# Kernel tuning notes

Hardware: AMD Instinct MI355X
Metric: run time of the kernel (lower is better)

## Reference

```python
import jax, jax.numpy as jnp
import numpy as np

B, CIN, COUT, R = 8, 256, 256, 128  # H = W = R (required by the module's permute-then-conv structure)


def _init_linear(key, out_c, in_c):
    # mimic torch Conv2d(kernel=1) default init: uniform(-1/sqrt(fan_in), 1/sqrt(fan_in))
    k1, k2 = jax.random.split(key)
    bound = 1.0 / np.sqrt(in_c)
    W = jax.random.uniform(k1, (out_c, in_c), jnp.float32, -bound, bound)
    b = jax.random.uniform(k2, (out_c,), jnp.float32, -bound, bound)
    return W, b


def setup_inputs() -> dict:
    key = jax.random.key(0)
    keys = jax.random.split(key, 9)
    x = jax.random.normal(keys[0], (B, CIN, R, R), jnp.float32)
    Wr, br = _init_linear(keys[1], R, CIN)          # resize conv
    Wqw, bqw = _init_linear(keys[2], R, R)          # width-attn q (mixes over H axis, H==R)
    Wkw, bkw = _init_linear(keys[3], R, R)
    Wvw, bvw = _init_linear(keys[4], R, R)
    Wqh, bqh = _init_linear(keys[5], R, R)          # height-attn q (mixes over W axis, W==R)
    Wkh, bkh = _init_linear(keys[6], R, R)
    Wvh, bvh = _init_linear(keys[7], R, R)
    Wo, bo = _init_linear(keys[8], COUT, R)         # restore conv
    return dict(x=x, Wr=Wr, br=br, Wqw=Wqw, bqw=bqw, Wkw=Wkw, bkw=bkw, Wvw=Wvw, bvw=bvw,
                Wqh=Wqh, bqh=bqh, Wkh=Wkh, bkh=bkh, Wvh=Wvh, bvh=bvh, Wo=Wo, bo=bo)


def _csaa_forward(x, Wr, br, Wqw, bqw, Wkw, bkw, Wvw, bvw, Wqh, bqh, Wkh, bkh, Wvh, bvh, Wo, bo):
    # resize 1x1 conv: [B,CIN,H,W] -> [B,R,H,W]
    resized = jnp.einsum('oc,bchw->bohw', Wr, x) + br[None, :, None, None]

    # --- width-branch AxialAttention (height_dim=False) ---
    # permute(0,2,1,3): [B,R,H,W] -> [B,H,R,W]; 1x1 conv now mixes over the H axis (H==R)
    xp = jnp.transpose(resized, (0, 2, 1, 3))                      # [B,H,R,W]
    q = jnp.einsum('oh,bhrw->borw', Wqw, xp) + bqw[None, :, None, None]
    k = jnp.einsum('oh,bhrw->borw', Wkw, xp) + bkw[None, :, None, None]
    v = jnp.einsum('oh,bhrw->borw', Wvw, xp) + bvw[None, :, None, None]
    attn = jax.nn.softmax(jnp.einsum('borw,bouw->boru', q, k), axis=-1)  # [B,O,R,R]
    out = jnp.einsum('boru,bouw->borw', attn, v)                   # [B,O,R,W]
    w_attn = jnp.transpose(out, (0, 2, 1, 3))                      # [B,R,O,W] == [B,R,H,W]

    # --- height-branch AxialAttention (height_dim=True) ---
    # permute(0,3,1,2): [B,R,H,W] -> [B,W,R,H]; 1x1 conv mixes over the W axis (W==R)
    xp = jnp.transpose(w_attn, (0, 3, 1, 2))                       # [B,W,R,H]
    q = jnp.einsum('ow,bwrh->borh', Wqh, xp) + bqh[None, :, None, None]
    k = jnp.einsum('ow,bwrh->borh', Wkh, xp) + bkh[None, :, None, None]
    v = jnp.einsum('ow,bwrh->borh', Wvh, xp) + bvh[None, :, None, None]
    attn = jax.nn.softmax(jnp.einsum('borh,bouh->boru', q, k), axis=-1)  # [B,O,R,R]
    out = jnp.einsum('boru,bouh->borh', attn, v)                   # [B,O,R,H]
    h_attn = jnp.transpose(out, (0, 2, 3, 1))                      # [B,R,H,O] == [B,R,H,W]

    # restore 1x1 conv: [B,R,H,W] -> [B,COUT,H,W]
    return jnp.einsum('oc,bchw->bohw', Wo, h_attn) + bo[None, :, None, None]


def reference(x, Wr, br, Wqw, bqw, Wkw, bkw, Wvw, bvw, Wqh, bqh, Wkh, bkh, Wvh, bvh, Wo, bo):
    return _csaa_forward(x, Wr, br, Wqw, bqw, Wkw, bkw, Wvw, bvw,
                         Wqh, bqh, Wkh, bkh, Wvh, bvh, Wo, bo)
```

## Files before the change

kernel.cpp:

```cpp
#include <hip/hip_runtime.h>
#include <hip/hip_bf16.h>


typedef __attribute__((ext_vector_type(8))) short bf16x8;
typedef __attribute__((ext_vector_type(4))) float f32x4;

__device__ __forceinline__ short f2b(float f) {
    __hip_bfloat16 h = __float2bfloat16(f);
    short s; __builtin_memcpy(&s, &h, 2);
    return s;
}

__device__ __forceinline__ int swx(int row) { return (row ^ (row >> 3)) & 7; }
__device__ __forceinline__ int swzb(int row, int blk) {
    return (row << 7) + ((blk ^ swx(row)) << 3);
}

__device__ __forceinline__ void gload16(const void* g, void* l) {
    __builtin_amdgcn_global_load_lds(
        (const __attribute__((address_space(1))) void*)g,
        (__attribute__((address_space(3))) void*)l, 16, 0, 0);
}

__device__ __forceinline__ void mfma_ag(const short* __restrict__ Ai,
                                        const short* __restrict__ Bs,
                                        f32x4 (&acc)[2][8], int lane, int wr) {
    #pragma unroll
    for (int kk = 0; kk < 4; kk++) {
        const int kb = kk * 4 + (lane >> 4);
        bf16x8 a[2];
        #pragma unroll
        for (int mi = 0; mi < 2; mi++)
            a[mi] = *(const bf16x8*)(Ai + kb * 1024
                                        + (wr + mi * 16 + (lane & 15)) * 8);
        #pragma unroll
        for (int nh = 0; nh < 2; nh++) {
            bf16x8 b[4];
            #pragma unroll
            for (int nj = 0; nj < 4; nj++)
                b[nj] = *(const bf16x8*)&Bs[swzb((nh * 4 + nj) * 16 + (lane & 15), kb)];
            #pragma unroll
            for (int mi = 0; mi < 2; mi++)
                #pragma unroll
                for (int nj = 0; nj < 4; nj++)
                    acc[mi][nh * 4 + nj] = __builtin_amdgcn_mfma_f32_16x16x32_bf16(
                        a[mi], b[nj], acc[mi][nh * 4 + nj], 0, 0, 0);
        }
    }
}

__device__ __forceinline__ void mfma16x128(const short* __restrict__ SA,
                                           const short* __restrict__ SB,
                                           f32x4 (&acc)[8], int lane, int wr16) {
    #pragma unroll
    for (int kk = 0; kk < 4; kk++) {
        const int kb = kk * 4 + (lane >> 4);
        bf16x8 a = *(const bf16x8*)&SA[swzb(wr16 + (lane & 15), kb)];
        #pragma unroll
        for (int nh = 0; nh < 2; nh++) {
            bf16x8 b[4];
            #pragma unroll
            for (int nj = 0; nj < 4; nj++)
                b[nj] = *(const bf16x8*)&SB[swzb((nh * 4 + nj) * 16 + (lane & 15), kb)];
            #pragma unroll
            for (int nj = 0; nj < 4; nj++)
                acc[nh * 4 + nj] = __builtin_amdgcn_mfma_f32_16x16x32_bf16(
                    a, b[nj], acc[nh * 4 + nj], 0, 0, 0);
        }
    }
}

__device__ __forceinline__ void mfma32x128(const short* __restrict__ SA,
                                           const short* __restrict__ SB,
                                           f32x4 (&acc)[2][8], int lane, int wr) {
    #pragma unroll
    for (int kk = 0; kk < 4; kk++) {
        const int kb = kk * 4 + (lane >> 4);
        bf16x8 a[2], b[8];
        #pragma unroll
        for (int mi = 0; mi < 2; mi++)
            a[mi] = *(const bf16x8*)&SA[swzb(wr + mi * 16 + (lane & 15), kb)];
        #pragma unroll
        for (int ni = 0; ni < 8; ni++)
            b[ni] = *(const bf16x8*)&SB[swzb(ni * 16 + (lane & 15), kb)];
        #pragma unroll
        for (int mi = 0; mi < 2; mi++)
            #pragma unroll
            for (int ni = 0; ni < 8; ni++)
                acc[mi][ni] = __builtin_amdgcn_mfma_f32_16x16x32_bf16(
                    a[mi], b[ni], acc[mi][ni], 0, 0, 0);
    }
}

__device__ __forceinline__ void stage_nf_bf16(const short* __restrict__ Bb,
                                              long long b_r, int k0,
                                              short* __restrict__ Bs, int t) {
    const int n8 = t & 15, kb = t >> 4;
    bf16x8 rk[8];
    #pragma unroll
    for (int i = 0; i < 8; i++)
        rk[i] = *(const bf16x8*)(Bb + (long long)(k0 + kb * 8 + i) * b_r + n8 * 8);
    #pragma unroll
    for (int j = 0; j < 8; j++) {
        bf16x8 col;
        #pragma unroll
        for (int i = 0; i < 8; i++) col[i] = rk[i][j];
        *(bf16x8*)&Bs[swzb(n8 * 8 + j, kb)] = col;
    }
}

__device__ __forceinline__ void stage_nf_f32(const float* __restrict__ Bb,
                                             long long b_r, int k0,
                                             short* __restrict__ Bs, int t) {
    const int n8 = t & 15, kb = t >> 4;
    bf16x8 rk[8];
    #pragma unroll
    for (int i = 0; i < 8; i++) {
        const float* s = Bb + (long long)(k0 + kb * 8 + i) * b_r + n8 * 8;
        float4 v0 = *(const float4*)s, v1 = *(const float4*)(s + 4);
        rk[i][0] = f2b(v0.x); rk[i][1] = f2b(v0.y);
        rk[i][2] = f2b(v0.z); rk[i][3] = f2b(v0.w);
        rk[i][4] = f2b(v1.x); rk[i][5] = f2b(v1.y);
        rk[i][6] = f2b(v1.z); rk[i][7] = f2b(v1.w);
    }
    #pragma unroll
    for (int j = 0; j < 8; j++) {
        bf16x8 col;
        #pragma unroll
        for (int i = 0; i < 8; i++) col[i] = rk[i][j];
        *(bf16x8*)&Bs[swzb(n8 * 8 + j, kb)] = col;
    }
}

__global__ __launch_bounds__(256)
void wprep(const float* __restrict__ Wr, const float* __restrict__ Wqw,
           const float* __restrict__ Wkw, const float* __restrict__ Wvw,
           const float* __restrict__ Wqh, const float* __restrict__ Wkh,
           const float* __restrict__ Wvh, const float* __restrict__ Wo,
           short* __restrict__ dst) {
    const int id = blockIdx.y;
    const float* W; int M, K, off;
    switch (id) {
        case 0: W = Wr;  M = 128; K = 256; off = 0;      break;
        case 1: W = Wqw; M = 128; K = 128; off = 32768;  break;
        case 2: W = Wkw; M = 128; K = 128; off = 49152;  break;
        case 3: W = Wvw; M = 128; K = 128; off = 65536;  break;
        case 4: W = Wqh; M = 128; K = 128; off = 81920;  break;
        case 5: W = Wkh; M = 128; K = 128; off = 98304;  break;
        case 6: W = Wvh; M = 128; K = 128; off = 114688; break;
        default: W = Wo; M = 256; K = 128; off = 131072; break;
    }
    int g = blockIdx.x * 256 + threadIdx.x;
    if (g >= (M * K) >> 3) return;
    int gpr = K >> 3;
    int row = g / gpr;
    int blk = g - row * gpr;
    int ks = blk >> 4, kb = blk & 15;
    int my = row >> 7, r = row & 127;
    int nks = K >> 7;
    const float* s = W + (long long)row * K + blk * 8;
    float4 v0 = *(const float4*)s, v1 = *(const float4*)(s + 4);
    bf16x8 ov;
    ov[0] = f2b(v0.x); ov[1] = f2b(v0.y); ov[2] = f2b(v0.z); ov[3] = f2b(v0.w);
    ov[4] = f2b(v1.x); ov[5] = f2b(v1.y); ov[6] = f2b(v1.z); ov[7] = f2b(v1.w);
    *(bf16x8*)(dst + off + ((my * nks + ks) * 16 + kb) * 1024 + r * 8) = ov;
}

__global__ __launch_bounds__(256, 4)
void gemm_p1(const short* __restrict__ A0, const float* __restrict__ bias0,
             const float* __restrict__ Bsrc,
             long long b_z, long long b_x, long long b_r,
             short* __restrict__ C0,
             long long c_z, long long c_x, long long c_m) {
    __shared__ short Bs[16384];
    const int t = threadIdx.x;
    const int lane = t & 63;
    const int wid = t >> 6;
    const int wr = wid * 32;
    const int bx = blockIdx.x, bz = blockIdx.z;

    f32x4 acc[2][8];
    #pragma unroll
    for (int mi = 0; mi < 2; mi++)
        #pragma unroll
        for (int ni = 0; ni < 8; ni++) acc[mi][ni] = (f32x4){0.f, 0.f, 0.f, 0.f};

    #pragma unroll
    for (int ks = 0; ks < 2; ks++) {
        if (ks) __syncthreads();
        stage_nf_f32(Bsrc + bz * b_z + bx * b_x, b_r, ks * 128, Bs, t);
        __syncthreads();
        mfma_ag(A0 + ks * 16384, Bs, acc, lane, wr);
    }
    __syncthreads();

    #pragma unroll
    for (int mi = 0; mi < 2; mi++)
        #pragma unroll
        for (int r = 0; r < 4; r++) {
            int row = wr + mi * 16 + (lane >> 4) * 4 + r;
            float bb = bias0[row];
            #pragma unroll
            for (int ni = 0; ni < 8; ni++) {
                int col = ni * 16 + (lane & 15);
                Bs[swzb(row, col >> 3) + (col & 7)] = f2b(acc[mi][ni][r] + bb);
            }
        }
    short* Cg = C0 + bz * c_z + bx * c_x;
    #pragma unroll
    for (int i = 0; i < 8; i++) {
        int idx = lane + i * 64;
        int row = wr + (idx >> 4), ch = idx & 15;
        *(bf16x8*)(Cg + (long long)row * c_m + ch * 8) =
            *(const bf16x8*)&Bs[swzb(row, ch)];
    }
}

template<int NW, int BMODE, bool F32OUT>
__global__ __launch_bounds__(256, 4)
void gemmu(const short* __restrict__ A0, const short* __restrict__ A1,
           const short* __restrict__ A2,
           const float* __restrict__ bias0, const float* __restrict__ bias1,
           const float* __restrict__ bias2,
           const void* __restrict__ Bsrc, long long b_z, long long b_x,
           long long b_r,
           short* __restrict__ C0, short* __restrict__ C1,
           short* __restrict__ C2, float* __restrict__ Cf,
           long long c_z, long long c_x, long long c_m) {
    __shared__ short Bs[16384];
    const int t = threadIdx.x;
    const int lane = t & 63;
    const int wid = t >> 6;
    const int wr = wid * 32;
    const int bx = blockIdx.x, gy = blockIdx.y, bz = blockIdx.z;

    const short* Ai;
    const float* bias;
    int myoff;
    if (NW > 1) {
        Ai = (gy == 0) ? A0 : (gy == 1) ? A1 : A2;
        bias = (gy == 0) ? bias0 : (gy == 1) ? bias1 : bias2;
        myoff = 0;
    } else {
        Ai = A0 + gy * 16384;
        bias = bias0;
        myoff = gy * 128;
    }

    if (BMODE == 0) {
        const short* Bb = (const short*)Bsrc + bz * b_z + bx * b_x;
        #pragma unroll
        for (int i = 0; i < 8; i++) {
            int q = wid * 8 + i;
            int row = q * 4 + (lane >> 4);
            gload16(Bb + (long long)row * b_r + (((lane & 15) ^ swx(row)) << 3),
                    &Bs[q * 512]);
        }
    } else {
        stage_nf_bf16((const short*)Bsrc + bz * b_z + bx * b_x, b_r, 0, Bs, t);
    }
    __syncthreads();

    f32x4 acc[2][8];
    #pragma unroll
    for (int mi = 0; mi < 2; mi++)
        #pragma unroll
        for (int ni = 0; ni < 8; ni++) acc[mi][ni] = (f32x4){0.f, 0.f, 0.f, 0.f};
    mfma_ag(Ai, Bs, acc, lane, wr);

    if (F32OUT) {
        float* Cb = Cf + bz * c_z + bx * c_x;
        #pragma unroll
        for (int mi = 0; mi < 2; mi++)
            #pragma unroll
            for (int r = 0; r < 4; r++) {
                int row = myoff + wr + mi * 16 + (lane >> 4) * 4 + r;
                float bb = bias[row];
                float* cp = Cb + (long long)row * c_m + (lane & 15);
                #pragma unroll
                for (int ni = 0; ni < 8; ni++)
                    cp[ni * 16] = acc[mi][ni][r] + bb;
            }
    } else {
        __syncthreads();
        #pragma unroll
        for (int mi = 0; mi < 2; mi++)
            #pragma unroll
            for (int r = 0; r < 4; r++) {
                int row = wr + mi * 16 + (lane >> 4) * 4 + r;
                float bb = bias[row];
                #pragma unroll
                for (int ni = 0; ni < 8; ni++) {
                    int col = ni * 16 + (lane & 15);
                    Bs[swzb(row, col >> 3) + (col & 7)] = f2b(acc[mi][ni][r] + bb);
                }
            }
        short* Cg = ((NW > 1) ? ((gy == 0) ? C0 : (gy == 1) ? C1 : C2) : C0)
                  + bz * c_z + bx * c_x;
        #pragma unroll
        for (int i = 0; i < 8; i++) {
            int idx = lane + i * 64;
            int row = wr + (idx >> 4), ch = idx & 15;
            *(bf16x8*)(Cg + (long long)row * c_m + ch * 8) =
                *(const bf16x8*)&Bs[swzb(row, ch)];
        }
    }
}

__global__ __launch_bounds__(256, 3)
void attnq(const short* __restrict__ Q, const short* __restrict__ Kp,
           const short* __restrict__ V, short* __restrict__ O) {
    __shared__ short SA[8192];
    __shared__ short SB[16384];
    const int t = threadIdx.x;
    const int lane = t & 63;
    const int wid = t >> 6;
    const int wr16 = wid * 16;
    const int o = blockIdx.x, qh = blockIdx.y, b = blockIdx.z;
    const long long poff = (long long)b * 2097152LL + (long long)o * 16384LL;
    const short* Qb = Q + poff + qh * 64 * 128;
    const short* Kb = Kp + poff;
    const short* Vb = V + poff;
    short* Ob = O + (long long)b * 2097152LL + (long long)o * 128LL
              + (long long)qh * 64 * 16384LL;

    #pragma unroll
    for (int i = 0; i < 4; i++) {
        int q = wid * 4 + i;
        int row = q * 4 + (lane >> 4);
        gload16(Qb + row * 128 + (((lane & 15) ^ swx(row)) << 3), &SA[q * 512]);
    }
    #pragma unroll
    for (int i = 0; i < 8; i++) {
        int q = wid * 8 + i;
        int row = q * 4 + (lane >> 4);
        gload16(Kb + row * 128 + (((lane & 15) ^ swx(row)) << 3), &SB[q * 512]);
    }
    const int n8 = t & 15, kb8 = t >> 4;
    bf16x8 vk[8];
    #pragma unroll
    for (int i = 0; i < 8; i++)
        vk[i] = *(const bf16x8*)(Vb + (kb8 * 8 + i) * 128 + n8 * 8);
    __syncthreads();

    f32x4 acc[8];
    #pragma unroll
    for (int ni = 0; ni < 8; ni++) acc[ni] = (f32x4){0.f, 0.f, 0.f, 0.f};
    mfma16x128(SA, SB, acc, lane, wr16);

    float rs[4];
    #pragma unroll
    for (int r = 0; r < 4; r++) {
        float mx = acc[0][r];
        #pragma unroll
        for (int ni = 1; ni < 8; ni++) mx = fmaxf(mx, acc[ni][r]);
        #pragma unroll
        for (int d = 1; d < 16; d <<= 1) mx = fmaxf(mx, __shfl_xor(mx, d, 64));
        float s = 0.f, p[8];
        #pragma unroll
        for (int ni = 0; ni < 8; ni++) {
            p[ni] = __expf(acc[ni][r] - mx);
            s += p[ni];
        }
        #pragma unroll
        for (int d = 1; d < 16; d <<= 1) s += __shfl_xor(s, d, 64);
        rs[r] = 1.f / s;
        int row = wr16 + (lane >> 4) * 4 + r;
        #pragma unroll
        for (int ni = 0; ni < 8; ni++) {
            int col = ni * 16 + (lane & 15);
            SA[swzb(row, col >> 3) + (col & 7)] = f2b(p[ni]);
        }
    }
    __syncthreads();

    #pragma unroll
    for (int j = 0; j < 8; j++) {
        bf16x8 col;
        #pragma unroll
        for (int i = 0; i < 8; i++) col[i] = vk[i][j];
        *(bf16x8*)&SB[swzb(n8 * 8 + j, kb8)] = col;
    }
    __syncthreads();

    f32x4 acc2[8];
    #pragma unroll
    for (int ni = 0; ni < 8; ni++) acc2[ni] = (f32x4){0.f, 0.f, 0.f, 0.f};
    mfma16x128(SA, SB, acc2, lane, wr16);

    #pragma unroll
    for (int r = 0; r < 4; r++) {
        int row = wr16 + (lane >> 4) * 4 + r;
        float rinv = rs[r];
        #pragma unroll
        for (int ni = 0; ni < 8; ni++) {
            int col = ni * 16 + (lane & 15);
            SA[swzb(row, col >> 3) + (col & 7)] = f2b(acc2[ni][r] * rinv);
        }
    }
    #pragma unroll
    for (int i = 0; i < 4; i++) {
        int idx = lane + i * 64;
        int row = wr16 + (idx >> 4), ch = idx & 15;
        *(bf16x8*)(Ob + (long long)row * 16384 + ch * 8) =
            *(const bf16x8*)&SA[swzb(row, ch)];
    }
}

template<bool TEPI>
__global__ __launch_bounds__(256)
void attnk(const short* __restrict__ Q, const short* __restrict__ Kp,
           const short* __restrict__ V, short* __restrict__ O) {
    __shared__ short SA[16384];
    __shared__ short SB[16384];
    const int t = threadIdx.x;
    const int lane = t & 63;
    const int wid = t >> 6;
    const int wr = wid * 32;
    const long long poff = (long long)blockIdx.z * 2097152LL
                         + (long long)blockIdx.x * 16384LL;
    const short* Qb = Q + poff;
    const short* Kb = Kp + poff;
    const short* Vb = V + poff;
    short* Ob = O + (long long)blockIdx.z * 2097152LL + (long long)blockIdx.x * 128LL;

    #pragma unroll
    for (int i = 0; i < 8; i++) {
        int q = wid * 8 + i;
        int row = q * 4 + (lane >> 4);
        int sw = (((lane & 15) ^ swx(row)) << 3);
        gload16(Qb + row * 128 + sw, &SA[q * 512]);
        gload16(Kb + row * 128 + sw, &SB[q * 512]);
    }
    const int n8 = t & 15, kb = t >> 4;
    bf16x8 vk[8];
    #pragma unroll
    for (int i = 0; i < 8; i++)
        vk[i] = *(const bf16x8*)(Vb + (kb * 8 + i) * 128 + n8 * 8);
    __syncthreads();

    f32x4 acc[2][8];
    #pragma unroll
    for (int mi = 0; mi < 2; mi++)
        #pragma unroll
        for (int ni = 0; ni < 8; ni++) acc[mi][ni] = (f32x4){0.f, 0.f, 0.f, 0.f};
    mfma32x128(SA, SB, acc, lane, wr);

    float rs[2][4];
    #pragma unroll
    for (int mi = 0; mi < 2; mi++)
        #pragma unroll
        for (int r = 0; r < 4; r++) {
            float mx = acc[mi][0][r];
            #pragma unroll
            for (int ni = 1; ni < 8; ni++) mx = fmaxf(mx, acc[mi][ni][r]);
            #pragma unroll
            for (int d = 1; d < 16; d <<= 1) mx = fmaxf(mx, __shfl_xor(mx, d, 64));
            float s = 0.f, p[8];
            #pragma unroll
            for (int ni = 0; ni < 8; ni++) {
                p[ni] = __expf(acc[mi][ni][r] - mx);
                s += p[ni];
            }
            #pragma unroll
            for (int d = 1; d < 16; d <<= 1) s += __shfl_xor(s, d, 64);
            rs[mi][r] = 1.f / s;
            int row = wr + mi * 16 + (lane >> 4) * 4 + r;
            #pragma unroll
            for (int ni = 0; ni < 8; ni++) {
                int col = ni * 16 + (lane & 15);
                SA[swzb(row, col >> 3) + (col & 7)] = f2b(p[ni]);
            }
        }
    __syncthreads();

    #pragma unroll
    for (int j = 0; j < 8; j++) {
        bf16x8 col;
        #pragma unroll
        for (int i = 0; i < 8; i++) col[i] = vk[i][j];
        *(bf16x8*)&SB[swzb(n8 * 8 + j, kb)] = col;
    }
    __syncthreads();

    f32x4 acc2[2][8];
    #pragma unroll
    for (int mi = 0; mi < 2; mi++)
        #pragma unroll
        for (int ni = 0; ni < 8; ni++) acc2[mi][ni] = (f32x4){0.f, 0.f, 0.f, 0.f};
    mfma32x128(SA, SB, acc2, lane, wr);

    if (!TEPI) {
        #pragma unroll
        for (int mi = 0; mi < 2; mi++)
            #pragma unroll
            for (int r = 0; r < 4; r++) {
                int row = wr + mi * 16 + (lane >> 4) * 4 + r;
                float rinv = rs[mi][r];
                #pragma unroll
                for (int ni = 0; ni < 8; ni++) {
                    int col = ni * 16 + (lane & 15);
                    SA[swzb(row, col >> 3) + (col & 7)] = f2b(acc2[mi][ni][r] * rinv);
                }
            }
        #pragma unroll
        for (int i = 0; i < 8; i++) {
            int idx = lane + i * 64;
            int row = wr + (idx >> 4), ch = idx & 15;
            *(bf16x8*)(Ob + (long long)row * 16384 + ch * 8) =
                *(const bf16x8*)&SA[swzb(row, ch)];
        }
    } else {
        __syncthreads();
        #pragma unroll
        for (int mi = 0; mi < 2; mi++)
            #pragma unroll
            for (int r = 0; r < 4; r++) {
                int row = wr + mi * 16 + (lane >> 4) * 4 + r;
                float rinv = rs[mi][r];
                #pragma unroll
                for (int ni = 0; ni < 8; ni++) {
                    int col = ni * 16 + (lane & 15);
                    SB[swzb(col, row >> 3) + (row & 7)] = f2b(acc2[mi][ni][r] * rinv);
                }
            }
        __syncthreads();
        #pragma unroll
        for (int i = 0; i < 8; i++) {
            int idx = t + i * 256;
            int row = idx >> 4, ch = idx & 15;
            *(bf16x8*)(Ob + (long long)row * 16384 + ch * 8) =
                *(const bf16x8*)&SB[swzb(row, ch)];
        }
    }
}

extern "C" void kernel_launch(void* const* d_in, const int* in_sizes, int n_in,
                              void* d_out, int out_size, void* d_ws, size_t ws_size,
                              hipStream_t stream) {
    const float* x   = (const float*)d_in[0];
    const float* Wr  = (const float*)d_in[1];
    const float* br  = (const float*)d_in[2];
    const float* Wqw = (const float*)d_in[3];
    const float* bqw = (const float*)d_in[4];
    const float* Wkw = (const float*)d_in[5];
    const float* bkw = (const float*)d_in[6];
    const float* Wvw = (const float*)d_in[7];
    const float* bvw = (const float*)d_in[8];
    const float* Wqh = (const float*)d_in[9];
    const float* bqh = (const float*)d_in[10];
    const float* Wkh = (const float*)d_in[11];
    const float* bkh = (const float*)d_in[12];
    const float* Wvh = (const float*)d_in[13];
    const float* bvh = (const float*)d_in[14];
    const float* Wo  = (const float*)d_in[15];
    const float* bo  = (const float*)d_in[16];
    float* out = (float*)d_out;
    (void)in_sizes; (void)n_in; (void)out_size; (void)ws_size;

    const long long U = 16777216LL;
    short* wsp = (short*)d_ws;
    short* s0 = wsp;
    short* s1 = wsp + U;
    short* s2 = wsp + 2 * U;
    short* s3 = wsp + 3 * U;
    short* wb = wsp + 4 * U;
    short* wWr  = wb;
    short* wWqw = wb + 32768;
    short* wWkw = wb + 49152;
    short* wWvw = wb + 65536;
    short* wWqh = wb + 81920;
    short* wWkh = wb + 98304;
    short* wWvh = wb + 114688;
    short* wWo  = wb + 131072;

    dim3 blk(256);

    wprep<<<dim3(16, 8), blk, 0, stream>>>(Wr, Wqw, Wkw, Wvw, Wqh, Wkh, Wvh, Wo, wb);

    gemm_p1<<<dim3(128, 1, 8), blk, 0, stream>>>(
        wWr, br, x, 4194304LL, 128LL, 16384LL,
        s0, 2097152LL, 128LL, 16384LL);

    gemmu<3, 1, false><<<dim3(128, 3, 8), blk, 0, stream>>>(
        wWqw, wWkw, wWvw, bqw, bkw, bvw,
        s0, 2097152LL, 16384LL, 128LL,
        s1, s2, s3, nullptr, 2097152LL, 128LL, 16384LL);

    attnq<<<dim3(128, 2, 8), blk, 0, stream>>>(s1, s2, s3, s0);

    gemmu<3, 0, false><<<dim3(128, 3, 8), blk, 0, stream>>>(
        wWqh, wWkh, wWvh, bqh, bkh, bvh,
        s0, 2097152LL, 16384LL, 128LL,
        s1, s2, s3, nullptr, 2097152LL, 128LL, 16384LL);

    attnk<true><<<dim3(128, 1, 8), blk, 0, stream>>>(s1, s2, s3, s0);

    gemmu<1, 0, true><<<dim3(128, 2, 8), blk, 0, stream>>>(
        wWo, nullptr, nullptr, bo, nullptr, nullptr,
        s0, 2097152LL, 16384LL, 128LL,
        nullptr, nullptr, nullptr, out, 4194304LL, 128LL, 16384LL);
}
```

Before: 224.0 us.

## Pre-transpose input to bf16 and route resize conv through generic GEMM

Adds a standalone transpose kernel that converts x from fp32 channel-major to a bf16 spatial-major layout, so the resize conv can use the generic gemmu path with async global-to-LDS loads over two K steps instead of the in-kernel fp32 transpose-and-convert staging. The gemmu kernel gains a K-step template parameter and an optional flattened grid that interleaves batch and Q/K/V weight slots. The non-transposed attention epilogue variant is removed. This adds an extra full pass over x (write and read of a bf16 copy) and more workspace in exchange for cheaper, better-coalesced staging in the first GEMM.

```diff
diff --git a/kernel.cpp b/kernel.cpp
--- a/kernel.cpp
+++ b/kernel.cpp
@@ -109,14 +109,21 @@
     }
 }
 
-__device__ __forceinline__ void stage_nf_f32(const float* __restrict__ Bb,
-                                             long long b_r, int k0,
-                                             short* __restrict__ Bs, int t) {
-    const int n8 = t & 15, kb = t >> 4;
+__global__ __launch_bounds__(256)
+void xpose2(const float* __restrict__ x, short* __restrict__ xt) {
+    const int t = threadIdx.x;
+    const int g = t >> 5;
+    const int h = t & 31;
+    const int hw0 = blockIdx.x * 256;
+    const int c0  = blockIdx.y * 64;
+    const long long boff = (long long)blockIdx.z * 4194304LL;
+    const float* xb = x + boff + (long long)(c0 + g * 8) * 16384 + hw0 + h * 8;
+    short* xtb = xt + boff + (long long)(hw0 + h * 8) * 256 + c0 + g * 8;
+
     bf16x8 rk[8];
     #pragma unroll
     for (int i = 0; i < 8; i++) {
-        const float* s = Bb + (long long)(k0 + kb * 8 + i) * b_r + n8 * 8;
+        const float* s = xb + (long long)i * 16384;
         float4 v0 = *(const float4*)s, v1 = *(const float4*)(s + 4);
         rk[i][0] = f2b(v0.x); rk[i][1] = f2b(v0.y);
         rk[i][2] = f2b(v0.z); rk[i][3] = f2b(v0.w);
@@ -128,7 +135,7 @@
         bf16x8 col;
         #pragma unroll
         for (int i = 0; i < 8; i++) col[i] = rk[i][j];
-        *(bf16x8*)&Bs[swzb(n8 * 8 + j, kb)] = col;
+        *(bf16x8*)(xtb + (long long)j * 256) = col;
     }
 }
 
@@ -166,57 +173,7 @@
     *(bf16x8*)(dst + off + ((my * nks + ks) * 16 + kb) * 1024 + r * 8) = ov;
 }
 
-__global__ __launch_bounds__(256, 4)
-void gemm_p1(const short* __restrict__ A0, const float* __restrict__ bias0,
-             const float* __restrict__ Bsrc,
-             long long b_z, long long b_x, long long b_r,
-             short* __restrict__ C0,
-             long long c_z, long long c_x, long long c_m) {
-    __shared__ short Bs[16384];
-    const int t = threadIdx.x;
-    const int lane = t & 63;
-    const int wid = t >> 6;
-    const int wr = wid * 32;
-    const int bx = blockIdx.x, bz = blockIdx.z;
-
-    f32x4 acc[2][8];
-    #pragma unroll
-    for (int mi = 0; mi < 2; mi++)
-        #pragma unroll
-        for (int ni = 0; ni < 8; ni++) acc[mi][ni] = (f32x4){0.f, 0.f, 0.f, 0.f};
-
-    #pragma unroll
-    for (int ks = 0; ks < 2; ks++) {
-        if (ks) __syncthreads();
-        stage_nf_f32(Bsrc + bz * b_z + bx * b_x, b_r, ks * 128, Bs, t);
-        __syncthreads();
-        mfma_ag(A0 + ks * 16384, Bs, acc, lane, wr);
-    }
-    __syncthreads();
-
-    #pragma unroll
-    for (int mi = 0; mi < 2; mi++)
-        #pragma unroll
-        for (int r = 0; r < 4; r++) {
-            int row = wr + mi * 16 + (lane >> 4) * 4 + r;
-            float bb = bias0[row];
-            #pragma unroll
-            for (int ni = 0; ni < 8; ni++) {
-                int col = ni * 16 + (lane & 15);
-                Bs[swzb(row, col >> 3) + (col & 7)] = f2b(acc[mi][ni][r] + bb);
-            }
-        }
-    short* Cg = C0 + bz * c_z + bx * c_x;
-    #pragma unroll
-    for (int i = 0; i < 8; i++) {
-        int idx = lane + i * 64;
-        int row = wr + (idx >> 4), ch = idx & 15;
-        *(bf16x8*)(Cg + (long long)row * c_m + ch * 8) =
-            *(const bf16x8*)&Bs[swzb(row, ch)];
-    }
-}
-
-template<int NW, int BMODE, bool F32OUT>
+template<int NW, int KSTEPS, int BMODE, bool F32OUT, bool XG>
 __global__ __launch_bounds__(256, 4)
 void gemmu(const short* __restrict__ A0, const short* __restrict__ A1,
            const short* __restrict__ A2,
@@ -232,41 +189,56 @@
     const int lane = t & 63;
     const int wid = t >> 6;
     const int wr = wid * 32;
-    const int bx = blockIdx.x, gy = blockIdx.y, bz = blockIdx.z;
-
-    const short* Ai;
+
+    int bx, bz, gy;
+    if (XG) {
+        int f = blockIdx.x;
+        bz = f & 7;
+        int slot = f >> 3;
+        gy = slot % 3;
+        bx = slot / 3;
+    } else {
+        bx = blockIdx.x; gy = blockIdx.y; bz = blockIdx.z;
+    }
+
+    const short* Abase;
     const float* bias;
     int myoff;
     if (NW > 1) {
-        Ai = (gy == 0) ? A0 : (gy == 1) ? A1 : A2;
+        Abase = (gy == 0) ? A0 : (gy == 1) ? A1 : A2;
         bias = (gy == 0) ? bias0 : (gy == 1) ? bias1 : bias2;
         myoff = 0;
     } else {
-        Ai = A0 + gy * 16384;
+        Abase = A0 + gy * (KSTEPS * 16384);
         bias = bias0;
         myoff = gy * 128;
     }
 
-    if (BMODE == 0) {
-        const short* Bb = (const short*)Bsrc + bz * b_z + bx * b_x;
-        #pragma unroll
-        for (int i = 0; i < 8; i++) {
-            int q = wid * 8 + i;
-            int row = q * 4 + (lane >> 4);
-            gload16(Bb + (long long)row * b_r + (((lane & 15) ^ swx(row)) << 3),
-                    &Bs[q * 512]);
-        }
-    } else {
-        stage_nf_bf16((const short*)Bsrc + bz * b_z + bx * b_x, b_r, 0, Bs, t);
-    }
-    __syncthreads();
-
     f32x4 acc[2][8];
     #pragma unroll
     for (int mi = 0; mi < 2; mi++)
         #pragma unroll
         for (int ni = 0; ni < 8; ni++) acc[mi][ni] = (f32x4){0.f, 0.f, 0.f, 0.f};
-    mfma_ag(Ai, Bs, acc, lane, wr);
+
+    #pragma unroll
+    for (int ks = 0; ks < KSTEPS; ks++) {
+        if (ks) __syncthreads();
+        if (BMODE == 0) {
+            const short* Bb = (const short*)Bsrc + bz * b_z + bx * b_x;
+            #pragma unroll
+            for (int i = 0; i < 8; i++) {
+                int q = wid * 8 + i;
+                int row = q * 4 + (lane >> 4);
+                gload16(Bb + (long long)row * b_r + ks * 128
+                           + (((lane & 15) ^ swx(row)) << 3), &Bs[q * 512]);
+            }
+        } else {
+            stage_nf_bf16((const short*)Bsrc + bz * b_z + bx * b_x, b_r,
+                          ks * 128, Bs, t);
+        }
+        __syncthreads();
+        mfma_ag(Abase + ks * 16384, Bs, acc, lane, wr);
+    }
 
     if (F32OUT) {
         float* Cb = Cf + bz * c_z + bx * c_x;
@@ -288,7 +260,7 @@
             #pragma unroll
             for (int r = 0; r < 4; r++) {
                 int row = wr + mi * 16 + (lane >> 4) * 4 + r;
-                float bb = bias[row];
+                float bb = bias[myoff + row];
                 #pragma unroll
                 for (int ni = 0; ni < 8; ni++) {
                     int col = ni * 16 + (lane & 15);
@@ -301,7 +273,7 @@
         for (int i = 0; i < 8; i++) {
             int idx = lane + i * 64;
             int row = wr + (idx >> 4), ch = idx & 15;
-            *(bf16x8*)(Cg + (long long)row * c_m + ch * 8) =
+            *(bf16x8*)(Cg + (long long)(myoff + row) * c_m + ch * 8) =
                 *(const bf16x8*)&Bs[swzb(row, ch)];
         }
     }
@@ -407,10 +379,9 @@
     }
 }
 
-template<bool TEPI>
 __global__ __launch_bounds__(256)
-void attnk(const short* __restrict__ Q, const short* __restrict__ Kp,
-           const short* __restrict__ V, short* __restrict__ O) {
+void attnk_t(const short* __restrict__ Q, const short* __restrict__ Kp,
+             const short* __restrict__ V, short* __restrict__ O) {
     __shared__ short SA[16384];
     __shared__ short SB[16384];
     const int t = threadIdx.x;
@@ -490,48 +461,26 @@
         for (int ni = 0; ni < 8; ni++) acc2[mi][ni] = (f32x4){0.f, 0.f, 0.f, 0.f};
     mfma32x128(SA, SB, acc2, lane, wr);
 
-    if (!TEPI) {
-        #pragma unroll
-        for (int mi = 0; mi < 2; mi++)
-            #pragma unroll
-            for (int r = 0; r < 4; r++) {
-                int row = wr + mi * 16 + (lane >> 4) * 4 + r;
-                float rinv = rs[mi][r];
-                #pragma unroll
-                for (int ni = 0; ni < 8; ni++) {
-                    int col = ni * 16 + (lane & 15);
-                    SA[swzb(row, col >> 3) + (col & 7)] = f2b(acc2[mi][ni][r] * rinv);
-                }
+    __syncthreads();
+    #pragma unroll
+    for (int mi = 0; mi < 2; mi++)
+        #pragma unroll
+        for (int r = 0; r < 4; r++) {
+            int row = wr + mi * 16 + (lane >> 4) * 4 + r;
+            float rinv = rs[mi][r];
+            #pragma unroll
+            for (int ni = 0; ni < 8; ni++) {
+                int col = ni * 16 + (lane & 15);
+                SB[swzb(col, row >> 3) + (row & 7)] = f2b(acc2[mi][ni][r] * rinv);
             }
-        #pragma unroll
-        for (int i = 0; i < 8; i++) {
-            int idx = lane + i * 64;
-            int row = wr + (idx >> 4), ch = idx & 15;
-            *(bf16x8*)(Ob + (long long)row * 16384 + ch * 8) =
-                *(const bf16x8*)&SA[swzb(row, ch)];
-        }
-    } else {
-        __syncthreads();
-        #pragma unroll
-        for (int mi = 0; mi < 2; mi++)
-            #pragma unroll
-            for (int r = 0; r < 4; r++) {
-                int row = wr + mi * 16 + (lane >> 4) * 4 + r;
-                float rinv = rs[mi][r];
-                #pragma unroll
-                for (int ni = 0; ni < 8; ni++) {
-                    int col = ni * 16 + (lane & 15);
-                    SB[swzb(col, row >> 3) + (row & 7)] = f2b(acc2[mi][ni][r] * rinv);
-                }
-            }
-        __syncthreads();
-        #pragma unroll
-        for (int i = 0; i < 8; i++) {
-            int idx = t + i * 256;
-            int row = idx >> 4, ch = idx & 15;
-            *(bf16x8*)(Ob + (long long)row * 16384 + ch * 8) =
-                *(const bf16x8*)&SB[swzb(row, ch)];
-        }
+        }
+    __syncthreads();
+    #pragma unroll
+    for (int i = 0; i < 8; i++) {
+        int idx = t + i * 256;
+        int row = idx >> 4, ch = idx & 15;
+        *(bf16x8*)(Ob + (long long)row * 16384 + ch * 8) =
+            *(const bf16x8*)&SB[swzb(row, ch)];
     }
 }
 
@@ -564,7 +513,8 @@
     short* s1 = wsp + U;
     short* s2 = wsp + 2 * U;
     short* s3 = wsp + 3 * U;
-    short* wb = wsp + 4 * U;
+    short* xt = wsp + 4 * U;
+    short* wb = wsp + 6 * U;
     short* wWr  = wb;
     short* wWqw = wb + 32768;
     short* wWkw = wb + 49152;
@@ -578,25 +528,28 @@
 
     wprep<<<dim3(16, 8), blk, 0, stream>>>(Wr, Wqw, Wkw, Wvw, Wqh, Wkh, Wvh, Wo, wb);
 
-    gemm_p1<<<dim3(128, 1, 8), blk, 0, stream>>>(
-        wWr, br, x, 4194304LL, 128LL, 16384LL,
-        s0, 2097152LL, 128LL, 16384LL);
-
-    gemmu<3, 1, false><<<dim3(128, 3, 8), blk, 0, stream>>>(
+    xpose2<<<dim3(64, 4, 8), blk, 0, stream>>>(x, xt);
+
+    gemmu<1, 2, 0, false, false><<<dim3(128, 1, 8), blk, 0, stream>>>(
+        wWr, nullptr, nullptr, br, nullptr, nullptr,
+        xt, 4194304LL, 32768LL, 256LL,
+        s0, nullptr, nullptr, nullptr, 2097152LL, 128LL, 16384LL);
+
+    gemmu<3, 1, 1, false, true><<<dim3(3072), blk, 0, stream>>>(
         wWqw, wWkw, wWvw, bqw, bkw, bvw,
         s0, 2097152LL, 16384LL, 128LL,
         s1, s2, s3, nullptr, 2097152LL, 128LL, 16384LL);
 
     attnq<<<dim3(128, 2, 8), blk, 0, stream>>>(s1, s2, s3, s0);
 
-    gemmu<3, 0, false><<<dim3(128, 3, 8), blk, 0, stream>>>(
+    gemmu<3, 1, 0, false, true><<<dim3(3072), blk, 0, stream>>>(
         wWqh, wWkh, wWvh, bqh, bkh, bvh,
         s0, 2097152LL, 16384LL, 128LL,
         s1, s2, s3, nullptr, 2097152LL, 128LL, 16384LL);
 
-    attnk<true><<<dim3(128, 1, 8), blk, 0, stream>>>(s1, s2, s3, s0);
-
-    gemmu<1, 0, true><<<dim3(128, 2, 8), blk, 0, stream>>>(
+    attnk_t<<<dim3(128, 1, 8), blk, 0, stream>>>(s1, s2, s3, s0);
+
+    gemmu<1, 1, 0, true, false><<<dim3(128, 2, 8), blk, 0, stream>>>(
         wWo, nullptr, nullptr, bo, nullptr, nullptr,
         s0, 2097152LL, 16384LL, 128LL,
         nullptr, nullptr, nullptr, out, 4194304LL, 128LL, 16384LL);
```

New measurement: 246.6 us. 10.1% more time.
